# Optimization experiments

Measured on AMD Instinct MI355X. Metric: run time of the kernel, lower is better.

## Reference

```python
import jax, jax.numpy as jnp
import numpy as np

NUM_USERS = 100000
NUM_ITEMS = 200000
EMBED_DIM = 128
NUM_EDGES = 2000000
N_LAYERS = 2
EPS = 1e-5


def layer_norm(x, gamma, beta):
    m = jnp.mean(x, axis=-1, keepdims=True)
    v = jnp.mean(jnp.square(x - m), axis=-1, keepdims=True)
    return gamma * (x - m) * jax.lax.rsqrt(v + EPS) + beta


def setup_inputs() -> dict:
    key = jax.random.key(0)
    k1, k2, k3, k4, k5 = jax.random.split(key, 5)
    user_emb = jax.random.normal(k1, (NUM_USERS, EMBED_DIM), dtype=jnp.float32) * 0.1
    item_emb = jax.random.normal(k2, (NUM_ITEMS, EMBED_DIM), dtype=jnp.float32) * 0.1
    # COO edge list for the user-item bipartite graph; iu_adj = ui_adj^T
    rows = jax.random.randint(k3, (NUM_EDGES,), 0, NUM_USERS, dtype=jnp.int32)
    cols = jax.random.randint(k4, (NUM_EDGES,), 0, NUM_ITEMS, dtype=jnp.int32)
    # positive normalized edge weights (e.g. sym-normalized adjacency values)
    vals = jax.random.uniform(k5, (NUM_EDGES,), dtype=jnp.float32) * (1.0 / 16.0)
    ln_gamma = jnp.ones((EMBED_DIM,), dtype=jnp.float32)
    ln_beta = jnp.zeros((EMBED_DIM,), dtype=jnp.float32)
    return {"user_emb": user_emb, "item_emb": item_emb, "vals": vals,
            "ln_gamma": ln_gamma, "ln_beta": ln_beta, "rows": rows, "cols": cols}


def reference(user_emb, item_emb, vals, ln_gamma, ln_beta, rows, cols):
    # SpMM via gather + segment_sum (COO). dropout is identity (eval / p=0).
    u_emb, i_emb = user_emb, item_emb
    for _ in range(N_LAYERS):
        # u_temp = ui_adj @ i_emb : [NUM_USERS, D]
        u_temp = jax.ops.segment_sum(vals[:, None] * i_emb[cols], rows,
                                     num_segments=NUM_USERS)
        # i_temp = iu_adj @ u_emb : [NUM_ITEMS, D]  (iu_adj = ui_adj^T)
        i_temp = jax.ops.segment_sum(vals[:, None] * u_emb[rows], cols,
                                     num_segments=NUM_ITEMS)
        u_emb = layer_norm(u_emb + u_temp, ln_gamma, ln_beta)
        i_emb = layer_norm(i_emb + i_temp, ln_gamma, ln_beta)
    return u_emb, i_emb
```

## Files before the change

### kernel.cpp

```cpp
#include <hip/hip_runtime.h>

#define EPS 1e-5f
typedef long long ll;
typedef unsigned int uint;
typedef float f32x2 __attribute__((ext_vector_type(2)));

#define CHUNK   8192
#define NCPAD   512
#define NBMAX   2048
#define P3CAP   8192

__device__ __forceinline__ uint bf_round(float x) {
    uint u = __float_as_uint(x);
    return (u + 0x7FFFu + ((u >> 16) & 1u)) >> 16;
}
__device__ __forceinline__ uint pack2(float a, float b) {
    return bf_round(a) | (bf_round(b) << 16);
}
__device__ __forceinline__ float unpack_lo(uint u) { return __uint_as_float(u << 16); }
__device__ __forceinline__ float unpack_hi(uint u) { return __uint_as_float(u & 0xFFFF0000u); }

__global__ __launch_bounds__(256) void hist_conv_k(
    const int* __restrict__ rows, const int* __restrict__ cols,
    int* __restrict__ counts, int ne, int nu, int NB, int hb,
    const float* __restrict__ ue, const float* __restrict__ ie,
    uint4* __restrict__ bfout, int nuT, int totT)
{
    int b = blockIdx.x;
    if (b < hb) {
        __shared__ int hist[NBMAX];
        for (int i = threadIdx.x; i < NB; i += 256) hist[i] = 0;
        __syncthreads();
        ll base0 = (ll)b * CHUNK;
        ll items = 2LL * ne;
        int n2 = (int)min((ll)CHUNK, items - base0);
        for (int k = threadIdx.x; k < n2; k += 256) {
            ll e = base0 + k;
            int bucket = (e < ne) ? rows[e] : nu + cols[e - ne];
            atomicAdd(&hist[bucket >> 8], 1);
        }
        __syncthreads();
        for (int i = threadIdx.x; i < NB; i += 256)
            counts[(ll)i * NCPAD + b] = hist[i];
    } else {
        int t = (b - hb) * 256 + threadIdx.x;
        if (t < totT) {
            const float4* src = (t < nuT) ? (const float4*)(ue + (ll)t * 8)
                                          : (const float4*)(ie + (ll)(t - nuT) * 8);
            float4 f0 = src[0], f1 = src[1];
            uint4 q;
            q.x = pack2(f0.x, f0.y); q.y = pack2(f0.z, f0.w);
            q.z = pack2(f1.x, f1.y); q.w = pack2(f1.z, f1.w);
            bfout[t] = q;
        }
    }
}

__global__ __launch_bounds__(256) void s1_kernel(
    const int* __restrict__ counts, int* __restrict__ base,
    int* __restrict__ binT, int nchunk)
{
    int b = blockIdx.x;
    int t = threadIdx.x;
    int i0 = 2 * t, i1 = 2 * t + 1;
    int v0 = (i0 < nchunk) ? counts[(ll)b * NCPAD + i0] : 0;
    int v1 = (i1 < nchunk) ? counts[(ll)b * NCPAD + i1] : 0;
    int s = v0 + v1;
    __shared__ int sm[256];
    sm[t] = s; __syncthreads();
    for (int off = 1; off < 256; off <<= 1) {
        int a = (t >= off) ? sm[t - off] : 0;
        __syncthreads();
        sm[t] += a;
        __syncthreads();
    }
    int excl = sm[t] - s;
    base[(ll)b * NCPAD + i0] = excl;
    base[(ll)b * NCPAD + i1] = excl + v0;
    if (t == 255) binT[b] = sm[255];
}

__global__ __launch_bounds__(256) void s2_kernel(
    const int* __restrict__ binT, int* __restrict__ binptr,
    int* __restrict__ rowptr, int NB, int Nrow, int total)
{
    __shared__ int sm[256];
    int t = threadIdx.x;
    const int PER = NBMAX / 256;
    int loc[PER]; int s = 0;
#pragma unroll
    for (int k = 0; k < PER; k++) {
        int i = t * PER + k;
        loc[k] = (i < NB) ? binT[i] : 0;
        s += loc[k];
    }
    sm[t] = s; __syncthreads();
    for (int off = 1; off < 256; off <<= 1) {
        int a = (t >= off) ? sm[t - off] : 0;
        __syncthreads();
        sm[t] += a;
        __syncthreads();
    }
    int run = sm[t] - s;
#pragma unroll
    for (int k = 0; k < PER; k++) {
        int i = t * PER + k;
        if (i < NB) binptr[i] = run;
        run += loc[k];
    }
    if (t == 0) { binptr[NB] = total; rowptr[Nrow] = total; }
}

__global__ __launch_bounds__(256) void p2_kernel(
    const int* __restrict__ rows, const int* __restrict__ cols,
    const float* __restrict__ vals,
    const int* __restrict__ base, const int* __restrict__ binptr,
    int2* __restrict__ tmp, int ne, int nu, int NB)
{
    __shared__ int cur[NBMAX];
    int c = blockIdx.x;
    for (int i = threadIdx.x; i < NB; i += 256)
        cur[i] = binptr[i] + base[(ll)i * NCPAD + c];
    __syncthreads();
    ll base0 = (ll)c * CHUNK;
    ll items = 2LL * ne;
    int n2 = (int)min((ll)CHUNK, items - base0);
    for (int k = threadIdx.x; k < n2; k += 256) {
        ll e = base0 + k;
        int bucket, src; float v;
        if (e < ne) { bucket = rows[e]; src = cols[e]; v = vals[e]; }
        else        { ll e2 = e - ne; bucket = nu + cols[e2]; src = rows[e2]; v = vals[e2]; }
        int slot = atomicAdd(&cur[bucket >> 8], 1);
        tmp[slot] = make_int2(((bucket & 255) << 24) | src, __float_as_int(v));
    }
}

__global__ __launch_bounds__(256) void p3_kernel(
    const int2* __restrict__ tmp, const int* __restrict__ binptr,
    int* __restrict__ rowptr, int2* __restrict__ csr)
{
    __shared__ int hist[256];
    __shared__ int sm[256];
    __shared__ int2 stage[P3CAP];
    int b = blockIdx.x;
    int t = threadIdx.x;
    int s0 = binptr[b], s1 = binptr[b + 1];
    int n = s1 - s0;
    bool inLds = (n <= P3CAP);
    hist[t] = 0; __syncthreads();
    if (inLds) {
        for (int i = t; i < n; i += 256) {
            int2 it = tmp[s0 + i];
            stage[i] = it;
            atomicAdd(&hist[(uint)it.x >> 24], 1);
        }
    } else {
        for (int i = t; i < n; i += 256)
            atomicAdd(&hist[(uint)tmp[s0 + i].x >> 24], 1);
    }
    __syncthreads();
    int v = hist[t];
    sm[t] = v; __syncthreads();
    for (int off = 1; off < 256; off <<= 1) {
        int a = (t >= off) ? sm[t - off] : 0;
        __syncthreads();
        sm[t] += a;
        __syncthreads();
    }
    int excl = sm[t] - v;
    __syncthreads();
    rowptr[(b << 8) + t] = s0 + excl;
    hist[t] = excl;
    __syncthreads();
    if (inLds) {
        for (int i = t; i < n; i += 256) {
            int2 it = stage[i];
            int r = atomicAdd(&hist[(uint)it.x >> 24], 1);
            csr[s0 + r] = make_int2(it.x & 0xFFFFFF, it.y);
        }
    } else {
        for (int i = t; i < n; i += 256) {
            int2 it = tmp[s0 + i];
            int r = atomicAdd(&hist[(uint)it.x >> 24], 1);
            csr[s0 + r] = make_int2(it.x & 0xFFFFFF, it.y);
        }
    }
}

template<bool OUT_BF>
__global__ __launch_bounds__(256) void gather_ln_k(
    const uint4* __restrict__ srcU, const uint4* __restrict__ srcI,
    const uint4* __restrict__ resU, const uint4* __restrict__ resI,
    void* __restrict__ outU, void* __restrict__ outI,
    const int* __restrict__ rowptr, const int2* __restrict__ csr,
    const float* __restrict__ gamma, const float* __restrict__ beta,
    int nu, int N)
{
    int w = blockIdx.x * 4 + (threadIdx.x >> 6);
    if (w >= N) return;
    int lane = threadIdx.x & 63;
    int sub  = lane >> 4;
    int l16  = lane & 15;

    const uint4* tbl;
    const uint4* res;
    void* out;
    if (w < nu) {
        tbl = srcU;
        res = resU + (ll)w * 16;
        out = OUT_BF ? (void*)((uint4*)outU + (ll)w * 16)
                     : (void*)((float4*)outU + (ll)w * 32);
    } else {
        int k = w - nu;
        tbl = srcI;
        res = resI + (ll)k * 16;
        out = OUT_BF ? (void*)((uint4*)outI + (ll)k * 16)
                     : (void*)((float4*)outI + (ll)k * 32);
    }

    int start = rowptr[w];
    int end   = rowptr[w + 1];

    f32x2 a01 = {0.f, 0.f}, a23 = {0.f, 0.f}, a45 = {0.f, 0.f}, a67 = {0.f, 0.f};

#define FMA8(q, vv) {                                                   \
        f32x2 b;                                                        \
        b[0] = unpack_lo(q.x); b[1] = unpack_hi(q.x); a01 = vv * b + a01; \
        b[0] = unpack_lo(q.y); b[1] = unpack_hi(q.y); a23 = vv * b + a23; \
        b[0] = unpack_lo(q.z); b[1] = unpack_hi(q.z); a45 = vv * b + a45; \
        b[0] = unpack_lo(q.w); b[1] = unpack_hi(q.w); a67 = vv * b + a67; }

    if (start < end) {
        int i0 = start + sub;
        int2 ecC = csr[i0 < end ? i0 : end - 1];
        int2 ecN = ecC;
        if (start + 4 < end) {
            int i1 = start + 4 + sub;
            ecN = csr[i1 < end ? i1 : end - 1];
        }
        uint4 qC = tbl[(((uint)ecC.x) << 4) + l16];

        int j = start;
        for (; j + 4 < end; j += 4) {
            int jnn = j + 8;
            int2 ecF = ecN;
            if (jnn < end) {
                int i2 = jnn + sub;
                ecF = csr[i2 < end ? i2 : end - 1];
            }
            uint4 qN = tbl[(((uint)ecN.x) << 4) + l16];
            float v = __int_as_float(ecC.y);
            f32x2 vv = {v, v};
            FMA8(qC, vv);
            ecC = ecN; ecN = ecF; qC = qN;
        }
        {
            float v = ((j + sub) < end) ? __int_as_float(ecC.y) : 0.0f;
            f32x2 vv = {v, v};
            FMA8(qC, vv);
        }
    }
#undef FMA8

    float a0 = a01[0], a1 = a01[1], a2 = a23[0], a3 = a23[1];
    float a4 = a45[0], a5 = a45[1], a6 = a67[0], a7 = a67[1];

#define MRG(x) x += __shfl_xor(x, 16, 64); x += __shfl_xor(x, 32, 64)
    MRG(a0); MRG(a1); MRG(a2); MRG(a3); MRG(a4); MRG(a5); MRG(a6); MRG(a7);
#undef MRG

    uint4 r = res[l16];
    a0 += unpack_lo(r.x); a1 += unpack_hi(r.x);
    a2 += unpack_lo(r.y); a3 += unpack_hi(r.y);
    a4 += unpack_lo(r.z); a5 += unpack_hi(r.z);
    a6 += unpack_lo(r.w); a7 += unpack_hi(r.w);

    float s  = a0+a1+a2+a3+a4+a5+a6+a7;
    float ss = a0*a0+a1*a1+a2*a2+a3*a3+a4*a4+a5*a5+a6*a6+a7*a7;
#pragma unroll
    for (int off = 8; off > 0; off >>= 1) {
        s  += __shfl_xor(s, off, 64);
        ss += __shfl_xor(ss, off, 64);
    }
    float m   = s * (1.0f / 128.0f);
    float var = ss * (1.0f / 128.0f) - m * m;
    float inv = rsqrtf(var + EPS);

    float4 g0 = ((const float4*)gamma)[l16 * 2];
    float4 g1 = ((const float4*)gamma)[l16 * 2 + 1];
    float4 b0 = ((const float4*)beta)[l16 * 2];
    float4 b1 = ((const float4*)beta)[l16 * 2 + 1];
    float o0 = g0.x * (a0 - m) * inv + b0.x;
    float o1 = g0.y * (a1 - m) * inv + b0.y;
    float o2 = g0.z * (a2 - m) * inv + b0.z;
    float o3 = g0.w * (a3 - m) * inv + b0.w;
    float o4 = g1.x * (a4 - m) * inv + b1.x;
    float o5 = g1.y * (a5 - m) * inv + b1.y;
    float o6 = g1.z * (a6 - m) * inv + b1.z;
    float o7 = g1.w * (a7 - m) * inv + b1.w;

    if (sub == 0) {
        if (OUT_BF) {
            uint4 q;
            q.x = pack2(o0, o1); q.y = pack2(o2, o3);
            q.z = pack2(o4, o5); q.w = pack2(o6, o7);
            ((uint4*)out)[l16] = q;
        } else {
            ((float4*)out)[l16 * 2]     = make_float4(o0, o1, o2, o3);
            ((float4*)out)[l16 * 2 + 1] = make_float4(o4, o5, o6, o7);
        }
    }
}

extern "C" void kernel_launch(void* const* d_in, const int* in_sizes, int n_in,
                              void* d_out, int out_size, void* d_ws, size_t ws_size,
                              hipStream_t stream)
{
    const float* user_emb = (const float*)d_in[0];
    const float* item_emb = (const float*)d_in[1];
    const float* vals     = (const float*)d_in[2];
    const float* gamma    = (const float*)d_in[3];
    const float* beta     = (const float*)d_in[4];
    const int*   rows     = (const int*)d_in[5];
    const int*   cols     = (const int*)d_in[6];

    const int nu = in_sizes[0] / 128;
    const int ni = in_sizes[1] / 128;
    const int ne = in_sizes[2];
    const int N  = nu + ni;
    const int total = 2 * ne;

    float* dout   = (float*)d_out;
    float* dout_u = dout;
    float* dout_i = dout + (ll)nu * 128;

    uint* bf_u = (uint*)d_out;
    uint* bf_i = bf_u + (ll)nu * 64;

    const int NB = (N + 255) >> 8;
    const int hb = (total + CHUNK - 1) / CHUNK;

    int*  rowptr  = (int*)d_ws;
    int*  counts  = rowptr + (ll)NB * 256;
    int*  base    = counts + (ll)NB * NCPAD;
    int*  binT    = base + (ll)NB * NCPAD;
    int*  binptr  = binT + NBMAX;
    int2* csr     = (int2*)(binptr + NBMAX);
    uint* wu_out  = (uint*)(csr + total);
    uint* wi_out  = wu_out + (ll)nu * 64;
    int2* tmp     = (int2*)wu_out;

    const int totT = (nu + ni) * 16;
    const int tb   = (totT + 255) / 256;

    hist_conv_k<<<hb + tb, 256, 0, stream>>>(rows, cols, counts, ne, nu, NB, hb,
                                             user_emb, item_emb,
                                             (uint4*)bf_u, nu * 16, totT);
    s1_kernel<<<NB, 256, 0, stream>>>(counts, base, binT, hb);
    s2_kernel<<<1, 256, 0, stream>>>(binT, binptr, rowptr, NB, N, total);
    p2_kernel<<<hb, 256, 0, stream>>>(rows, cols, vals, base, binptr, tmp, ne, nu, NB);
    p3_kernel<<<NB, 256, 0, stream>>>(tmp, binptr, rowptr, csr);

    const int gblocks = (N + 3) / 4;

    gather_ln_k<true><<<gblocks, 256, 0, stream>>>(
        (const uint4*)bf_i, (const uint4*)bf_u,
        (const uint4*)bf_u, (const uint4*)bf_i,
        wu_out, wi_out,
        rowptr, csr, gamma, beta, nu, N);

    gather_ln_k<false><<<gblocks, 256, 0, stream>>>(
        (const uint4*)wi_out, (const uint4*)wu_out,
        (const uint4*)wu_out, (const uint4*)wi_out,
        dout_u, dout_i,
        rowptr, csr, gamma, beta, nu, N);
}
```

Baseline: 741.9 us.

## Map one row per 16-lane group in gather-LN and shrink sort chunks

The gather+layernorm kernel now assigns four rows per wavefront, one per 16-lane subgroup, instead of splitting one row's edges across four subgroups. This drops the cross-subgroup shuffle merge and lets every lane write output. The loop runs to the maximum degree in the wave and masks shorter rows, so rows of uneven degree can leave lanes idle. Separately, the sort chunk size is halved with a doubled count padding, and the scan kernel now handles four counts per thread using int4 loads and stores.

```diff
diff --git a/kernel.cpp b/kernel.cpp
--- a/kernel.cpp
+++ b/kernel.cpp
@@ -5,8 +5,8 @@
 typedef unsigned int uint;
 typedef float f32x2 __attribute__((ext_vector_type(2)));
 
-#define CHUNK   8192
-#define NCPAD   512
+#define CHUNK   4096
+#define NCPAD   1024
 #define NBMAX   2048
 #define P3CAP   8192
 
@@ -62,10 +62,13 @@
 {
     int b = blockIdx.x;
     int t = threadIdx.x;
-    int i0 = 2 * t, i1 = 2 * t + 1;
-    int v0 = (i0 < nchunk) ? counts[(ll)b * NCPAD + i0] : 0;
-    int v1 = (i1 < nchunk) ? counts[(ll)b * NCPAD + i1] : 0;
-    int s = v0 + v1;
+    int4 v = ((const int4*)(counts + (ll)b * NCPAD))[t];
+    int i0 = 4 * t;
+    if (i0 + 0 >= nchunk) v.x = 0;
+    if (i0 + 1 >= nchunk) v.y = 0;
+    if (i0 + 2 >= nchunk) v.z = 0;
+    if (i0 + 3 >= nchunk) v.w = 0;
+    int s = v.x + v.y + v.z + v.w;
     __shared__ int sm[256];
     sm[t] = s; __syncthreads();
     for (int off = 1; off < 256; off <<= 1) {
@@ -75,8 +78,9 @@
         __syncthreads();
     }
     int excl = sm[t] - s;
-    base[(ll)b * NCPAD + i0] = excl;
-    base[(ll)b * NCPAD + i1] = excl + v0;
+    int4 o;
+    o.x = excl; o.y = o.x + v.x; o.z = o.y + v.y; o.w = o.z + v.z;
+    ((int4*)(base + (ll)b * NCPAD))[t] = o;
     if (t == 255) binT[b] = sm[255];
 }
 
@@ -189,37 +193,46 @@
 
 template<bool OUT_BF>
 __global__ __launch_bounds__(256) void gather_ln_k(
-    const uint4* __restrict__ srcU, const uint4* __restrict__ srcI,
+    const uint4* __restrict__ srcU,
+    const uint4* __restrict__ srcI,
     const uint4* __restrict__ resU, const uint4* __restrict__ resI,
     void* __restrict__ outU, void* __restrict__ outI,
     const int* __restrict__ rowptr, const int2* __restrict__ csr,
     const float* __restrict__ gamma, const float* __restrict__ beta,
     int nu, int N)
 {
-    int w = blockIdx.x * 4 + (threadIdx.x >> 6);
-    if (w >= N) return;
+    int gw = blockIdx.x * 4 + (threadIdx.x >> 6);
+    if (gw * 4 >= N) return;
     int lane = threadIdx.x & 63;
     int sub  = lane >> 4;
     int l16  = lane & 15;
 
+    int row = gw * 4 + sub;
+    bool rv = row < N;
+    int rowc = rv ? row : N - 1;
+
+    int start = rv ? rowptr[row]     : 0;
+    int end   = rv ? rowptr[row + 1] : 0;
+    int deg   = end - start;
+    int md = deg;
+    md = max(md, __shfl_xor(md, 16, 64));
+    md = max(md, __shfl_xor(md, 32, 64));
+
     const uint4* tbl;
     const uint4* res;
-    void* out;
-    if (w < nu) {
-        tbl = srcU;
-        res = resU + (ll)w * 16;
-        out = OUT_BF ? (void*)((uint4*)outU + (ll)w * 16)
-                     : (void*)((float4*)outU + (ll)w * 32);
+    char* outp;
+    if (rowc < nu) {
+        tbl  = srcU;
+        res  = resU + (ll)rowc * 16;
+        outp = OUT_BF ? (char*)outU + (ll)rowc * 256
+                      : (char*)outU + (ll)rowc * 512;
     } else {
-        int k = w - nu;
-        tbl = srcI;
-        res = resI + (ll)k * 16;
-        out = OUT_BF ? (void*)((uint4*)outI + (ll)k * 16)
-                     : (void*)((float4*)outI + (ll)k * 32);
-    }
-
-    int start = rowptr[w];
-    int end   = rowptr[w + 1];
+        int k = rowc - nu;
+        tbl  = srcI;
+        res  = resI + (ll)k * 16;
+        outp = OUT_BF ? (char*)outI + (ll)k * 256
+                      : (char*)outI + (ll)k * 512;
+    }
 
     f32x2 a01 = {0.f, 0.f}, a23 = {0.f, 0.f}, a45 = {0.f, 0.f}, a67 = {0.f, 0.f};
 
@@ -230,44 +243,23 @@
         b[0] = unpack_lo(q.z); b[1] = unpack_hi(q.z); a45 = vv * b + a45; \
         b[0] = unpack_lo(q.w); b[1] = unpack_hi(q.w); a67 = vv * b + a67; }
 
-    if (start < end) {
-        int i0 = start + sub;
-        int2 ecC = csr[i0 < end ? i0 : end - 1];
-        int2 ecN = ecC;
-        if (start + 4 < end) {
-            int i1 = start + 4 + sub;
-            ecN = csr[i1 < end ? i1 : end - 1];
-        }
-        uint4 qC = tbl[(((uint)ecC.x) << 4) + l16];
-
-        int j = start;
-        for (; j + 4 < end; j += 4) {
-            int jnn = j + 8;
-            int2 ecF = ecN;
-            if (jnn < end) {
-                int i2 = jnn + sub;
-                ecF = csr[i2 < end ? i2 : end - 1];
-            }
-            uint4 qN = tbl[(((uint)ecN.x) << 4) + l16];
-            float v = __int_as_float(ecC.y);
-            f32x2 vv = {v, v};
-            FMA8(qC, vv);
-            ecC = ecN; ecN = ecF; qC = qN;
-        }
-        {
-            float v = ((j + sub) < end) ? __int_as_float(ecC.y) : 0.0f;
-            f32x2 vv = {v, v};
-            FMA8(qC, vv);
+    if (md > 0) {
+        int2 ec0 = csr[(0 < deg) ? start     : 0];
+        int2 ec1 = csr[(1 < deg) ? start + 1 : 0];
+        uint4 q0 = tbl[(((uint)ec0.x) << 4) + l16];
+        for (int k = 0; k < md; ++k) {
+            int2 ec2 = csr[((k + 2) < deg) ? (start + k + 2) : 0];
+            uint4 q1 = tbl[(((uint)ec1.x) << 4) + l16];
+            float vm = (k < deg) ? __int_as_float(ec0.y) : 0.0f;
+            f32x2 vv = {vm, vm};
+            FMA8(q0, vv);
+            ec0 = ec1; ec1 = ec2; q0 = q1;
         }
     }
 #undef FMA8
 
     float a0 = a01[0], a1 = a01[1], a2 = a23[0], a3 = a23[1];
     float a4 = a45[0], a5 = a45[1], a6 = a67[0], a7 = a67[1];
-
-#define MRG(x) x += __shfl_xor(x, 16, 64); x += __shfl_xor(x, 32, 64)
-    MRG(a0); MRG(a1); MRG(a2); MRG(a3); MRG(a4); MRG(a5); MRG(a6); MRG(a7);
-#undef MRG
 
     uint4 r = res[l16];
     a0 += unpack_lo(r.x); a1 += unpack_hi(r.x);
@@ -299,15 +291,15 @@
     float o6 = g1.z * (a6 - m) * inv + b1.z;
     float o7 = g1.w * (a7 - m) * inv + b1.w;
 
-    if (sub == 0) {
+    if (rv) {
         if (OUT_BF) {
             uint4 q;
             q.x = pack2(o0, o1); q.y = pack2(o2, o3);
             q.z = pack2(o4, o5); q.w = pack2(o6, o7);
-            ((uint4*)out)[l16] = q;
+            ((uint4*)outp)[l16] = q;
         } else {
-            ((float4*)out)[l16 * 2]     = make_float4(o0, o1, o2, o3);
-            ((float4*)out)[l16 * 2 + 1] = make_float4(o4, o5, o6, o7);
+            ((float4*)outp)[l16 * 2]     = make_float4(o0, o1, o2, o3);
+            ((float4*)outp)[l16 * 2 + 1] = make_float4(o4, o5, o6, o7);
         }
     }
 }
@@ -361,7 +353,7 @@
     p2_kernel<<<hb, 256, 0, stream>>>(rows, cols, vals, base, binptr, tmp, ne, nu, NB);
     p3_kernel<<<NB, 256, 0, stream>>>(tmp, binptr, rowptr, csr);
 
-    const int gblocks = (N + 3) / 4;
+    const int gblocks = (N + 15) / 16;
 
     gather_ln_k<true><<<gblocks, 256, 0, stream>>>(
         (const uint4*)bf_i, (const uint4*)bf_u,
```

Result: faster. 693.5 us (-6.5%).
